# Kernel tuning notes

Measured on AMD Instinct MI355X. Metric: run time of the kernel, lower is better.

Reference implementation:

```python
import jax, jax.numpy as jnp
import numpy as np

NUM_HEADS = 8
NEG_SLOPE = 0.2


def typed_linear(x, W, etype):
    # x: [E, din], W: [T, din, dout], etype: [E] int. Grouped (per-edge-type) linear,
    # computed as T dense GEMMs with a per-edge select (T is small and static).
    out = jnp.zeros((x.shape[0], W.shape[2]), x.dtype)
    for t in range(W.shape[0]):
        out = out + jnp.where((etype == t)[:, None], x @ W[t], jnp.zeros((), x.dtype))
    return out


def setup_inputs() -> dict:
    key = jax.random.key(0)
    ks = jax.random.split(key, 9)
    N, E, IN = 50000, 800000, 128
    H, D = NUM_HEADS, 16
    HD = H * D  # 128
    T = 8  # num edge types
    s = 0.05
    return {
        "x": jax.random.normal(ks[0], (N, IN), jnp.float32),
        "src": jax.random.randint(ks[1], (E,), 0, N),
        "dst": jax.random.randint(ks[2], (E,), 0, N),
        "etype": jax.random.randint(ks[3], (E,), 0, T),
        "W_w": jax.random.normal(ks[4], (T, IN, HD), jnp.float32) * s,
        "W_al": jax.random.normal(ks[5], (T, HD, HD), jnp.float32) * s,
        "W_ar": jax.random.normal(ks[6], (T, HD, HD), jnp.float32) * s,
        "W_res": jax.random.normal(ks[7], (IN, HD), jnp.float32) * s,
        "b_res": jnp.zeros((HD,), jnp.float32),
    }


def reference(x, src, dst, etype, W_w, W_al, W_ar, W_res, b_res):
    N = x.shape[0]
    HD = W_w.shape[2]
    H = NUM_HEADS
    D = HD // H

    m = x[src]                                   # copy_u gather: [E, in]
    feat = typed_linear(m, W_w, etype)           # [E, H*D]
    h = feat                                     # dropout p=0 (eval/deterministic)

    # per-head attention logits
    h_l = typed_linear(h, W_al, etype).reshape(-1, H, D).sum(-1)  # [E, H]
    h_r = typed_linear(h, W_ar, etype).reshape(-1, H, D).sum(-1)  # [E, H]
    att = jax.nn.leaky_relu(h_l + h_r, NEG_SLOPE)

    # edge_softmax: segment softmax over incoming edges of each dst node
    att_max = jax.ops.segment_max(att, dst, num_segments=N)       # [N, H]
    att_exp = jnp.exp(att - att_max[dst])
    denom = jax.ops.segment_sum(att_exp, dst, num_segments=N)
    att = att_exp / denom[dst]                                    # [E, H]

    # NOTE: in the original source, 'alpha' is computed and stored in edata but the
    # aggregation copies edata 'm' (== h), so alpha never reaches the output.
    alpha = jnp.einsum('ehd,eh->ed', h.reshape(-1, H, D), att)    # [E, D] (dead)
    del alpha

    # update_all(copy_e('m'), sum): scatter-sum of h into dst nodes
    emb = jax.ops.segment_sum(h, dst, num_segments=N)             # [N, H*D]

    out = emb + x @ W_res + b_res                                 # residual
    return jax.nn.elu(out)
```

## Files before the change

kernel.cpp:

```cpp
#include <hip/hip_runtime.h>
#include <hip/hip_bf16.h>


#define KW 1152
#define CAP 6144
#define CHUNK 4096

typedef __bf16 bf16x8 __attribute__((ext_vector_type(8)));
typedef float f32x4 __attribute__((ext_vector_type(4)));

__device__ __forceinline__ void gload_lds16(const void* g, void* l) {
  __builtin_amdgcn_global_load_lds(
      (const __attribute__((address_space(1))) unsigned int*)g,
      (__attribute__((address_space(3))) unsigned int*)l, 16, 0, 0);
}

__global__ __launch_bounds__(256) void k_binA(
    const int* __restrict__ src, const int* __restrict__ dst,
    const int* __restrict__ et, int* __restrict__ gCount,
    int* __restrict__ bucketBuf, int E) {
  __shared__ int buf[CHUNK];
  __shared__ unsigned char bkt[CHUNK];
  __shared__ int hist[256], sc[256], ls[256], cur[256], gb[256];
  const int tid = threadIdx.x;
  const int base = blockIdx.x * CHUNK;
  const int cnt = min(CHUNK, E - base);

  hist[tid] = 0;
  __syncthreads();
  for (int j = tid; j < cnt; j += 256) atomicAdd(&hist[dst[base + j] >> 8], 1);
  __syncthreads();
  sc[tid] = hist[tid];
  __syncthreads();
  for (int off = 1; off < 256; off <<= 1) {
    int t = (tid >= off) ? sc[tid - off] : 0;
    __syncthreads();
    if (tid >= off) sc[tid] += t;
    __syncthreads();
  }
  ls[tid] = sc[tid] - hist[tid];
  cur[tid] = ls[tid];
  gb[tid] = (hist[tid] > 0) ? atomicAdd(&gCount[tid], hist[tid]) : 0;
  __syncthreads();
  for (int j = tid; j < cnt; j += 256) {
    int e = base + j;
    int d = dst[e];
    int b = d >> 8;
    int pos = atomicAdd(&cur[b], 1);
    buf[pos] = (src[e] << 11) | (et[e] << 8) | (d & 255);
    bkt[pos] = (unsigned char)b;
  }
  __syncthreads();
  for (int j = tid; j < cnt; j += 256) {
    int b = bkt[j];
    bucketBuf[b * CAP + gb[b] + (j - ls[b])] = buf[j];
  }
}

__global__ __launch_bounds__(256) void k_scanC(
    const int* __restrict__ gCount, int* __restrict__ coarseBase,
    int* __restrict__ rowstart, int N, int E) {
  __shared__ int sc[256], h[256];
  int tid = threadIdx.x;
  h[tid] = gCount[tid];
  sc[tid] = h[tid];
  __syncthreads();
  for (int off = 1; off < 256; off <<= 1) {
    int t = (tid >= off) ? sc[tid - off] : 0;
    __syncthreads();
    if (tid >= off) sc[tid] += t;
    __syncthreads();
  }
  coarseBase[tid] = sc[tid] - h[tid];
  if (tid == 0) rowstart[N] = E;
}

__global__ __launch_bounds__(256) void k_sortB(
    const int* __restrict__ bucketBuf, const int* __restrict__ gCount,
    const int* __restrict__ coarseBase, int* __restrict__ rowstart,
    int* __restrict__ packed, int N) {
  __shared__ int raw[CAP];
  __shared__ int srt[CAP];
  __shared__ int hist[256], sc[256], bs[256], cur[256];
  const int b = blockIdx.x;
  const int tid = threadIdx.x;
  const int cnt = min(gCount[b], CAP);
  const int base = coarseBase[b];

  hist[tid] = 0;
  __syncthreads();
  for (int j = tid; j < cnt; j += 256) {
    int p = bucketBuf[b * CAP + j];
    raw[j] = p;
    atomicAdd(&hist[p & 255], 1);
  }
  __syncthreads();
  sc[tid] = hist[tid];
  __syncthreads();
  for (int off = 1; off < 256; off <<= 1) {
    int t = (tid >= off) ? sc[tid - off] : 0;
    __syncthreads();
    if (tid >= off) sc[tid] += t;
    __syncthreads();
  }
  bs[tid] = sc[tid] - hist[tid];
  cur[tid] = bs[tid];
  int node = b * 256 + tid;
  if (node < N) rowstart[node] = base + bs[tid];
  __syncthreads();
  for (int j = tid; j < cnt; j += 256) {
    int p = raw[j];
    int pos = atomicAdd(&cur[p & 255], 1);
    srt[pos] = p;
  }
  __syncthreads();
  for (int j = tid; j < cnt; j += 256) {
    int p = srt[j];
    packed[base + j] = (p >> 11) * 576 + (((p >> 8) & 7) << 6);
  }
}

__global__ void k_xcast(const float* __restrict__ x, __hip_bfloat16* __restrict__ xb,
                        int n, int npad) {
  int i = blockIdx.x * 256 + threadIdx.x;
  if (i < npad) xb[i] = __float2bfloat16(i < n ? x[i] : 0.f);
}

__global__ void k_wb(const float* __restrict__ Ww, const float* __restrict__ Wres,
                     __hip_bfloat16* __restrict__ Wb) {
  int o = blockIdx.x * 256 + threadIdx.x;
  if (o >= KW * 128) return;
  int nn = o >> 7, kk = o & 127;
  float v = (nn < 1024) ? Ww[(nn >> 7) * 16384 + kk * 128 + (nn & 127)]
                        : Wres[kk * 128 + (nn & 127)];
  Wb[o] = __float2bfloat16(v);
}

__global__ __launch_bounds__(512) void k_ygemm(
    const __hip_bfloat16* __restrict__ xb, const __hip_bfloat16* __restrict__ Wb,
    __hip_bfloat16* __restrict__ y) {
  __shared__ __align__(16) unsigned short As[128 * 128];
  __shared__ __align__(16) unsigned short Bs[128 * 128];
  const int tid = threadIdx.x;
  const int lane = tid & 63;
  const int wid = tid >> 6;
  const int wr = wid >> 2, wc = wid & 3;
  const long row0 = (long)blockIdx.x * 128;
  const int nb0 = blockIdx.y * 128;

  const char* xbb = (const char*)xb;
  const char* wbb = (const char*)Wb;
  char* asb = (char*)As;
  char* bsb = (char*)Bs;

#pragma unroll
  for (int i = 0; i < 8; ++i) {
    int c = i * 512 + tid;
    int half = c >> 11;
    int cc = c & 2047;
    int r = cc >> 4, colb = (cc & 15) << 4;
    int srcb = colb ^ ((r & 7) << 4);
    if (half == 0)
      gload_lds16(xbb + (row0 + r) * 256 + srcb, asb + r * 256 + colb);
    else
      gload_lds16(wbb + (long)(nb0 + r) * 256 + srcb, bsb + r * 256 + colb);
  }
  asm volatile("s_waitcnt vmcnt(0)" ::: "memory");
  __syncthreads();

  f32x4 acc[4][2] = {};
#pragma unroll
  for (int ks = 0; ks < 4; ++ks) {
    const int cb = ks * 64 + ((lane >> 4) << 4);
    bf16x8 af[4], bfr[2];
#pragma unroll
    for (int mi = 0; mi < 4; ++mi) {
      int row = wr * 64 + mi * 16 + (lane & 15);
      af[mi] = *(const bf16x8*)(asb + ((row * 256 + cb) ^ ((row & 7) << 4)));
    }
#pragma unroll
    for (int ni = 0; ni < 2; ++ni) {
      int rowb = wc * 32 + ni * 16 + (lane & 15);
      bfr[ni] = *(const bf16x8*)(bsb + ((rowb * 256 + cb) ^ ((rowb & 7) << 4)));
    }
#pragma unroll
    for (int mi = 0; mi < 4; ++mi)
#pragma unroll
      for (int ni = 0; ni < 2; ++ni)
        acc[mi][ni] = __builtin_amdgcn_mfma_f32_16x16x32_bf16(
            af[mi], bfr[ni], acc[mi][ni], 0, 0, 0);
  }

#pragma unroll
  for (int mi = 0; mi < 4; ++mi)
#pragma unroll
    for (int ni = 0; ni < 2; ++ni) {
      int col = nb0 + wc * 32 + ni * 16 + (lane & 15);
      long rb = row0 + wr * 64 + mi * 16 + ((lane >> 4) << 2);
      f32x4 v = acc[mi][ni];
#pragma unroll
      for (int q = 0; q < 4; ++q)
        y[(rb + q) * KW + col] = __float2bfloat16(v[q]);
    }
}

__global__ __launch_bounds__(256) void k_scat(
    const ushort2* __restrict__ y2, const int* __restrict__ rowstart,
    const int* __restrict__ packed, const float* __restrict__ bres,
    float* __restrict__ out, int N) {
  const int w = threadIdx.x >> 6, lane = threadIdx.x & 63;
  const int n = blockIdx.x * 4 + w;
  if (n >= N) return;
  float ax = 0.f, ay = 0.f;
  int e = rowstart[n];
  const int end = rowstart[n + 1];
  for (; e + 16 <= end; e += 16) {
    int p[16];
#pragma unroll
    for (int j = 0; j < 16; ++j) p[j] = packed[e + j];
    ushort2 r[16];
#pragma unroll
    for (int j = 0; j < 16; ++j) r[j] = y2[p[j] + lane];
#pragma unroll
    for (int j = 0; j < 16; ++j) {
      ax += __uint_as_float((unsigned)r[j].x << 16);
      ay += __uint_as_float((unsigned)r[j].y << 16);
    }
  }
  for (; e + 4 <= end; e += 4) {
    int p[4];
#pragma unroll
    for (int j = 0; j < 4; ++j) p[j] = packed[e + j];
    ushort2 r[4];
#pragma unroll
    for (int j = 0; j < 4; ++j) r[j] = y2[p[j] + lane];
#pragma unroll
    for (int j = 0; j < 4; ++j) {
      ax += __uint_as_float((unsigned)r[j].x << 16);
      ay += __uint_as_float((unsigned)r[j].y << 16);
    }
  }
  for (; e < end; ++e) {
    ushort2 r = y2[packed[e] + lane];
    ax += __uint_as_float((unsigned)r.x << 16);
    ay += __uint_as_float((unsigned)r.y << 16);
  }
  ushort2 rr = y2[n * 576 + 512 + lane];
  ax += __uint_as_float((unsigned)rr.x << 16) + bres[2 * lane];
  ay += __uint_as_float((unsigned)rr.y << 16) + bres[2 * lane + 1];
  float2 o;
  o.x = ax > 0.f ? ax : (expf(ax) - 1.f);
  o.y = ay > 0.f ? ay : (expf(ay) - 1.f);
  *(float2*)(out + (long)n * 128 + 2 * lane) = o;
}

extern "C" void kernel_launch(void* const* d_in, const int* in_sizes, int n_in,
                              void* d_out, int out_size, void* d_ws, size_t ws_size,
                              hipStream_t stream) {
  const float* x = (const float*)d_in[0];
  const int* src = (const int*)d_in[1];
  const int* dst = (const int*)d_in[2];
  const int* et = (const int*)d_in[3];
  const float* Ww = (const float*)d_in[4];
  const float* Wres = (const float*)d_in[7];
  const float* bres = (const float*)d_in[8];
  float* out = (float*)d_out;

  const int N = in_sizes[0] / 128;
  const int E = in_sizes[1];
  const int padM = ((N + 127) / 128) * 128;
  const int COARSE = (N + 255) >> 8;

  char* ws = (char*)d_ws;
  size_t off = 0;
  auto take = [&](size_t b) {
    char* p = ws + off;
    off = (off + b + 255) & ~(size_t)255;
    return p;
  };
  __hip_bfloat16* y = (__hip_bfloat16*)take((size_t)padM * KW * 2);
  __hip_bfloat16* Wb = (__hip_bfloat16*)take((size_t)KW * 128 * 2);
  __hip_bfloat16* xb = (__hip_bfloat16*)take((size_t)padM * 128 * 2);
  int* rowstart = (int*)take((size_t)(N + 1) * 4);
  int* gCount = (int*)take(256 * 4);
  int* coarseBase = (int*)take(256 * 4);
  int* packed = (int*)take((size_t)E * 4);
  int* bucketBuf = (int*)y;

  hipMemsetAsync(gCount, 0, 256 * 4, stream);
  k_binA<<<(E + CHUNK - 1) / CHUNK, 256, 0, stream>>>(src, dst, et, gCount, bucketBuf, E);
  k_scanC<<<1, 256, 0, stream>>>(gCount, coarseBase, rowstart, N, E);
  k_sortB<<<COARSE, 256, 0, stream>>>(bucketBuf, gCount, coarseBase, rowstart, packed, N);
  k_wb<<<(KW * 128 + 255) / 256, 256, 0, stream>>>(Ww, Wres, Wb);
  k_xcast<<<(padM * 128 + 255) / 256, 256, 0, stream>>>(x, xb, N * 128, padM * 128);
  dim3 gy(padM / 128, 9);
  k_ygemm<<<gy, 512, 0, stream>>>(xb, Wb, y);
  k_scat<<<(N + 3) / 4, 256, 0, stream>>>((const ushort2*)y, rowstart, packed, bres, out, N);
}
```

Measured before the change: 207.7 us.

## Use finer 128-node sort buckets, vectorize x cast, add nontemporal stores and sched barriers

The two-pass counting sort now uses 512 coarse buckets of 128 nodes each, with 512-thread blocks and smaller chunks. The goal is more sort blocks with less shared memory per block. The x-to-bf16 cast now works on four floats per thread. The GEMM output and the final output use nontemporal stores, and the scatter loop gets scheduling barriers so all gathers issue before the adds. The src field loses one bit of shift headroom, and the fixed bucket capacity CAP of 3072 per bucket still holds for this input's degree distribution.

```diff
diff --git a/kernel.cpp b/kernel.cpp
--- a/kernel.cpp
+++ b/kernel.cpp
@@ -3,11 +3,12 @@
 
 
 #define KW 1152
-#define CAP 6144
-#define CHUNK 4096
+#define CAP 3072
+#define CHUNK 2048
 
 typedef __bf16 bf16x8 __attribute__((ext_vector_type(8)));
 typedef float f32x4 __attribute__((ext_vector_type(4)));
+typedef float f32x2 __attribute__((ext_vector_type(2)));
 
 __device__ __forceinline__ void gload_lds16(const void* g, void* l) {
   __builtin_amdgcn_global_load_lds(
@@ -15,24 +16,24 @@
       (__attribute__((address_space(3))) unsigned int*)l, 16, 0, 0);
 }
 
-__global__ __launch_bounds__(256) void k_binA(
+__global__ __launch_bounds__(512) void k_binA(
     const int* __restrict__ src, const int* __restrict__ dst,
     const int* __restrict__ et, int* __restrict__ gCount,
     int* __restrict__ bucketBuf, int E) {
   __shared__ int buf[CHUNK];
-  __shared__ unsigned char bkt[CHUNK];
-  __shared__ int hist[256], sc[256], ls[256], cur[256], gb[256];
+  __shared__ short bkt[CHUNK];
+  __shared__ int hist[512], sc[512], ls[512], cur[512], gb[512];
   const int tid = threadIdx.x;
   const int base = blockIdx.x * CHUNK;
   const int cnt = min(CHUNK, E - base);
 
   hist[tid] = 0;
   __syncthreads();
-  for (int j = tid; j < cnt; j += 256) atomicAdd(&hist[dst[base + j] >> 8], 1);
+  for (int j = tid; j < cnt; j += 512) atomicAdd(&hist[dst[base + j] >> 7], 1);
   __syncthreads();
   sc[tid] = hist[tid];
   __syncthreads();
-  for (int off = 1; off < 256; off <<= 1) {
+  for (int off = 1; off < 512; off <<= 1) {
     int t = (tid >= off) ? sc[tid - off] : 0;
     __syncthreads();
     if (tid >= off) sc[tid] += t;
@@ -42,30 +43,30 @@
   cur[tid] = ls[tid];
   gb[tid] = (hist[tid] > 0) ? atomicAdd(&gCount[tid], hist[tid]) : 0;
   __syncthreads();
-  for (int j = tid; j < cnt; j += 256) {
+  for (int j = tid; j < cnt; j += 512) {
     int e = base + j;
     int d = dst[e];
-    int b = d >> 8;
+    int b = d >> 7;
     int pos = atomicAdd(&cur[b], 1);
-    buf[pos] = (src[e] << 11) | (et[e] << 8) | (d & 255);
-    bkt[pos] = (unsigned char)b;
-  }
-  __syncthreads();
-  for (int j = tid; j < cnt; j += 256) {
+    buf[pos] = (src[e] << 10) | (et[e] << 7) | (d & 127);
+    bkt[pos] = (short)b;
+  }
+  __syncthreads();
+  for (int j = tid; j < cnt; j += 512) {
     int b = bkt[j];
     bucketBuf[b * CAP + gb[b] + (j - ls[b])] = buf[j];
   }
 }
 
-__global__ __launch_bounds__(256) void k_scanC(
+__global__ __launch_bounds__(512) void k_scanC(
     const int* __restrict__ gCount, int* __restrict__ coarseBase,
     int* __restrict__ rowstart, int N, int E) {
-  __shared__ int sc[256], h[256];
+  __shared__ int sc[512], h[512];
   int tid = threadIdx.x;
   h[tid] = gCount[tid];
   sc[tid] = h[tid];
   __syncthreads();
-  for (int off = 1; off < 256; off <<= 1) {
+  for (int off = 1; off < 512; off <<= 1) {
     int t = (tid >= off) ? sc[tid - off] : 0;
     __syncthreads();
     if (tid >= off) sc[tid] += t;
@@ -75,55 +76,66 @@
   if (tid == 0) rowstart[N] = E;
 }
 
-__global__ __launch_bounds__(256) void k_sortB(
+__global__ __launch_bounds__(512) void k_sortB(
     const int* __restrict__ bucketBuf, const int* __restrict__ gCount,
     const int* __restrict__ coarseBase, int* __restrict__ rowstart,
     int* __restrict__ packed, int N) {
   __shared__ int raw[CAP];
   __shared__ int srt[CAP];
-  __shared__ int hist[256], sc[256], bs[256], cur[256];
+  __shared__ int hist[128], sc[128], bs[128], cur[128];
   const int b = blockIdx.x;
   const int tid = threadIdx.x;
   const int cnt = min(gCount[b], CAP);
   const int base = coarseBase[b];
 
-  hist[tid] = 0;
-  __syncthreads();
-  for (int j = tid; j < cnt; j += 256) {
+  if (tid < 128) hist[tid] = 0;
+  __syncthreads();
+  for (int j = tid; j < cnt; j += 512) {
     int p = bucketBuf[b * CAP + j];
     raw[j] = p;
-    atomicAdd(&hist[p & 255], 1);
-  }
-  __syncthreads();
-  sc[tid] = hist[tid];
-  __syncthreads();
-  for (int off = 1; off < 256; off <<= 1) {
-    int t = (tid >= off) ? sc[tid - off] : 0;
-    __syncthreads();
-    if (tid >= off) sc[tid] += t;
-    __syncthreads();
-  }
-  bs[tid] = sc[tid] - hist[tid];
-  cur[tid] = bs[tid];
-  int node = b * 256 + tid;
-  if (node < N) rowstart[node] = base + bs[tid];
-  __syncthreads();
-  for (int j = tid; j < cnt; j += 256) {
+    atomicAdd(&hist[p & 127], 1);
+  }
+  __syncthreads();
+  if (tid < 128) sc[tid] = hist[tid];
+  __syncthreads();
+  for (int off = 1; off < 128; off <<= 1) {
+    int t = (tid < 128 && tid >= off) ? sc[tid - off] : 0;
+    __syncthreads();
+    if (tid < 128 && tid >= off) sc[tid] += t;
+    __syncthreads();
+  }
+  if (tid < 128) {
+    bs[tid] = sc[tid] - hist[tid];
+    cur[tid] = bs[tid];
+    int node = b * 128 + tid;
+    if (node < N) rowstart[node] = base + bs[tid];
+  }
+  __syncthreads();
+  for (int j = tid; j < cnt; j += 512) {
     int p = raw[j];
-    int pos = atomicAdd(&cur[p & 255], 1);
+    int pos = atomicAdd(&cur[p & 127], 1);
     srt[pos] = p;
   }
   __syncthreads();
-  for (int j = tid; j < cnt; j += 256) {
+  for (int j = tid; j < cnt; j += 512) {
     int p = srt[j];
-    packed[base + j] = (p >> 11) * 576 + (((p >> 8) & 7) << 6);
-  }
-}
-
-__global__ void k_xcast(const float* __restrict__ x, __hip_bfloat16* __restrict__ xb,
-                        int n, int npad) {
+    packed[base + j] = (p >> 10) * 576 + (((p >> 7) & 7) << 6);
+  }
+}
+
+__global__ void k_xcast(const float* __restrict__ x, ushort4* __restrict__ xb4,
+                        int n4, int npad4) {
   int i = blockIdx.x * 256 + threadIdx.x;
-  if (i < npad) xb[i] = __float2bfloat16(i < n ? x[i] : 0.f);
+  if (i >= npad4) return;
+  ushort4 o = {0, 0, 0, 0};
+  if (i < n4) {
+    f32x4 v = *(const f32x4*)(x + i * 4);
+    __hip_bfloat16 h0 = __float2bfloat16(v[0]), h1 = __float2bfloat16(v[1]);
+    __hip_bfloat16 h2 = __float2bfloat16(v[2]), h3 = __float2bfloat16(v[3]);
+    o.x = *(unsigned short*)&h0; o.y = *(unsigned short*)&h1;
+    o.z = *(unsigned short*)&h2; o.w = *(unsigned short*)&h3;
+  }
+  xb4[i] = o;
 }
 
 __global__ void k_wb(const float* __restrict__ Ww, const float* __restrict__ Wres,
@@ -138,7 +150,7 @@
 
 __global__ __launch_bounds__(512) void k_ygemm(
     const __hip_bfloat16* __restrict__ xb, const __hip_bfloat16* __restrict__ Wb,
-    __hip_bfloat16* __restrict__ y) {
+    unsigned short* __restrict__ y) {
   __shared__ __align__(16) unsigned short As[128 * 128];
   __shared__ __align__(16) unsigned short Bs[128 * 128];
   const int tid = threadIdx.x;
@@ -199,8 +211,10 @@
       long rb = row0 + wr * 64 + mi * 16 + ((lane >> 4) << 2);
       f32x4 v = acc[mi][ni];
 #pragma unroll
-      for (int q = 0; q < 4; ++q)
-        y[(rb + q) * KW + col] = __float2bfloat16(v[q]);
+      for (int q = 0; q < 4; ++q) {
+        __hip_bfloat16 h = __float2bfloat16(v[q]);
+        __builtin_nontemporal_store(*(unsigned short*)&h, y + (rb + q) * KW + col);
+      }
     }
 }
 
@@ -221,23 +235,27 @@
     ushort2 r[16];
 #pragma unroll
     for (int j = 0; j < 16; ++j) r[j] = y2[p[j] + lane];
+    __builtin_amdgcn_sched_barrier(0);
 #pragma unroll
     for (int j = 0; j < 16; ++j) {
       ax += __uint_as_float((unsigned)r[j].x << 16);
       ay += __uint_as_float((unsigned)r[j].y << 16);
     }
   }
-  for (; e + 4 <= end; e += 4) {
+  {
     int p[4];
-#pragma unroll
-    for (int j = 0; j < 4; ++j) p[j] = packed[e + j];
     ushort2 r[4];
-#pragma unroll
-    for (int j = 0; j < 4; ++j) r[j] = y2[p[j] + lane];
-#pragma unroll
-    for (int j = 0; j < 4; ++j) {
-      ax += __uint_as_float((unsigned)r[j].x << 16);
-      ay += __uint_as_float((unsigned)r[j].y << 16);
+    for (; e + 4 <= end; e += 4) {
+#pragma unroll
+      for (int j = 0; j < 4; ++j) p[j] = packed[e + j];
+#pragma unroll
+      for (int j = 0; j < 4; ++j) r[j] = y2[p[j] + lane];
+      __builtin_amdgcn_sched_barrier(0);
+#pragma unroll
+      for (int j = 0; j < 4; ++j) {
+        ax += __uint_as_float((unsigned)r[j].x << 16);
+        ay += __uint_as_float((unsigned)r[j].y << 16);
+      }
     }
   }
   for (; e < end; ++e) {
@@ -248,10 +266,10 @@
   ushort2 rr = y2[n * 576 + 512 + lane];
   ax += __uint_as_float((unsigned)rr.x << 16) + bres[2 * lane];
   ay += __uint_as_float((unsigned)rr.y << 16) + bres[2 * lane + 1];
-  float2 o;
-  o.x = ax > 0.f ? ax : (expf(ax) - 1.f);
-  o.y = ay > 0.f ? ay : (expf(ay) - 1.f);
-  *(float2*)(out + (long)n * 128 + 2 * lane) = o;
+  f32x2 o;
+  o[0] = ax > 0.f ? ax : (expf(ax) - 1.f);
+  o[1] = ay > 0.f ? ay : (expf(ay) - 1.f);
+  __builtin_nontemporal_store(o, (f32x2*)(out + (long)n * 128 + 2 * lane));
 }
 
 extern "C" void kernel_launch(void* const* d_in, const int* in_sizes, int n_in,
@@ -269,7 +287,7 @@
   const int N = in_sizes[0] / 128;
   const int E = in_sizes[1];
   const int padM = ((N + 127) / 128) * 128;
-  const int COARSE = (N + 255) >> 8;
+  const int COARSE = (N + 127) >> 7;
 
   char* ws = (char*)d_ws;
   size_t off = 0;
@@ -282,18 +300,19 @@
   __hip_bfloat16* Wb = (__hip_bfloat16*)take((size_t)KW * 128 * 2);
   __hip_bfloat16* xb = (__hip_bfloat16*)take((size_t)padM * 128 * 2);
   int* rowstart = (int*)take((size_t)(N + 1) * 4);
-  int* gCount = (int*)take(256 * 4);
-  int* coarseBase = (int*)take(256 * 4);
+  int* gCount = (int*)take(512 * 4);
+  int* coarseBase = (int*)take(512 * 4);
   int* packed = (int*)take((size_t)E * 4);
   int* bucketBuf = (int*)y;
 
-  hipMemsetAsync(gCount, 0, 256 * 4, stream);
-  k_binA<<<(E + CHUNK - 1) / CHUNK, 256, 0, stream>>>(src, dst, et, gCount, bucketBuf, E);
-  k_scanC<<<1, 256, 0, stream>>>(gCount, coarseBase, rowstart, N, E);
-  k_sortB<<<COARSE, 256, 0, stream>>>(bucketBuf, gCount, coarseBase, rowstart, packed, N);
+  hipMemsetAsync(gCount, 0, 512 * 4, stream);
+  k_binA<<<(E + CHUNK - 1) / CHUNK, 512, 0, stream>>>(src, dst, et, gCount, bucketBuf, E);
+  k_scanC<<<1, 512, 0, stream>>>(gCount, coarseBase, rowstart, N, E);
+  k_sortB<<<COARSE, 512, 0, stream>>>(bucketBuf, gCount, coarseBase, rowstart, packed, N);
   k_wb<<<(KW * 128 + 255) / 256, 256, 0, stream>>>(Ww, Wres, Wb);
-  k_xcast<<<(padM * 128 + 255) / 256, 256, 0, stream>>>(x, xb, N * 128, padM * 128);
+  const int n4 = N * 128 / 4, npad4 = padM * 128 / 4;
+  k_xcast<<<(npad4 + 255) / 256, 256, 0, stream>>>(x, (ushort4*)xb, n4, npad4);
   dim3 gy(padM / 128, 9);
-  k_ygemm<<<gy, 512, 0, stream>>>(xb, Wb, y);
+  k_ygemm<<<gy, 512, 0, stream>>>(xb, Wb, (unsigned short*)y);
   k_scat<<<(N + 3) / 4, 256, 0, stream>>>((const ushort2*)y, rowstart, packed, bres, out, N);
 }
```

After: 220.5 us. 6.2% more time.
